# Kernel tuning notes

Hardware: AMD Instinct MI355X
Metric: run time of the kernel (lower is better)

Reference implementation:

```python
import jax, jax.numpy as jnp
import numpy as np

N = 100000           # nodes
E = 1600000          # directed edges (avg degree 16)
G = 64               # graphs in batch


def gcn_conv(x, src, dst, ew, W, b, n):
    """PyG GCNConv with edge weights and self-loops already appended.

    out[i] = sum_{(j->i)} d[j]^-1/2 * ew * d[i]^-1/2 * (x W)[j] + b
    where d[i] = sum of incoming edge weights at i (incl. self-loop).
    """
    xw = x @ W                                               # [n, out]
    deg = jax.ops.segment_sum(ew, dst, num_segments=n)       # [n]
    dinv = jnp.where(deg > 0, jax.lax.rsqrt(deg), 0.0)
    norm = dinv[src] * ew * dinv[dst]                        # [e]
    msg = xw[src] * norm[:, None]                            # [e, out] gather
    out = jax.ops.segment_sum(msg, dst, num_segments=n)      # scatter-add
    return out + b


def setup_inputs() -> dict:
    key = jax.random.key(0)
    ks = jax.random.split(key, 10)
    x = jax.random.normal(ks[0], (N, 256), dtype=jnp.float32)
    edge_index = jax.random.randint(ks[1], (2, E), 0, N, dtype=jnp.int64)
    edge_weight = jax.random.uniform(ks[2], (E,), dtype=jnp.float32)
    batch = jnp.sort(jax.random.randint(ks[3], (N,), 0, G, dtype=jnp.int64))
    s = 0.05
    W1 = jax.random.normal(ks[4], (256, 128), dtype=jnp.float32) * s
    b1 = jnp.zeros((128,), dtype=jnp.float32)
    W2 = jax.random.normal(ks[5], (128, 64), dtype=jnp.float32) * s
    b2 = jnp.zeros((64,), dtype=jnp.float32)
    Wfc = jax.random.normal(ks[6], (64, 1), dtype=jnp.float32) * s
    bfc = jnp.zeros((1,), dtype=jnp.float32)
    return {"x": x, "edge_index": edge_index, "edge_weight": edge_weight,
            "batch": batch, "W1": W1, "b1": b1, "W2": W2, "b2": b2,
            "Wfc": Wfc, "bfc": bfc}


def reference(x, edge_index, edge_weight, batch, W1, b1, W2, b2, Wfc, bfc):
    n = x.shape[0]
    loop = jnp.arange(n, dtype=edge_index.dtype)
    src = jnp.concatenate([edge_index[0], loop])             # add self-loops
    dst = jnp.concatenate([edge_index[1], loop])
    ew = jnp.concatenate([edge_weight, jnp.ones((n,), x.dtype)])

    h = jax.nn.relu(gcn_conv(x, src, dst, ew, W1, b1, n))    # [N,128]
    h = jax.nn.relu(gcn_conv(h, src, dst, ew, W2, b2, n))    # [N,64]

    # global_mean_pool over batch ids
    sums = jax.ops.segment_sum(h, batch, num_segments=G)     # [G,64]
    cnt = jax.ops.segment_sum(jnp.ones((n,), h.dtype), batch, num_segments=G)
    pooled = sums / jnp.maximum(cnt, 1.0)[:, None]
    return pooled @ Wfc + bfc                                # [G,1]
```

## Files before the change

kernel.cpp:

```cpp
#include <hip/hip_runtime.h>
#include <hip/hip_bf16.h>


static inline int ceil_div_ll(long long a, int b) { return (int)((a + b - 1) / b); }

typedef __attribute__((ext_vector_type(8))) short bf16x8;
typedef __attribute__((ext_vector_type(4))) float f32x4;

#define FIX_SCALE 33554432.0f

__device__ inline unsigned short f2bf(float f) {
    __hip_bfloat16 h = __float2bfloat16(f);
    return *reinterpret_cast<unsigned short*>(&h);
}
__device__ inline float bf2f(unsigned short u) {
    unsigned int x = ((unsigned int)u) << 16;
    return __uint_as_float(x);
}

__global__ void k_init_pk(unsigned long long* __restrict__ pk, int n) {
    int i = blockIdx.x * blockDim.x + threadIdx.x;
    if (i < n) pk[i] = (unsigned long long)(1u << 25);
}

__global__ void k_deg_count(const int* __restrict__ dst, const float* __restrict__ ew,
                            unsigned long long* __restrict__ pk, int* __restrict__ slot, int E) {
    int e = blockIdx.x * blockDim.x + threadIdx.x;
    if (e < E) {
        unsigned int fx = __float2uint_rn(ew[e] * FIX_SCALE);
        unsigned long long old =
            atomicAdd(&pk[dst[e]], (1ull << 32) | (unsigned long long)fx);
        slot[e] = (int)(old >> 32);
    }
}

__global__ void k_finish(const unsigned long long* __restrict__ pk, float* __restrict__ dinv,
                         int* __restrict__ count, int n) {
    int i = blockIdx.x * blockDim.x + threadIdx.x;
    if (i < n) {
        unsigned long long v = pk[i];
        float deg = (float)(unsigned int)(v & 0xffffffffull) * (1.0f / FIX_SCALE);
        dinv[i] = (deg > 0.f) ? rsqrtf(deg) : 0.f;
        count[i] = (int)(v >> 32);
    }
}

constexpr int SC_T = 256;
constexpr int SC_PER = 16;
constexpr int SC_CHUNK = SC_T * SC_PER;

__global__ void k_scan_a(const int* __restrict__ count, int* __restrict__ bsum, int n) {
    __shared__ int lds[SC_T];
    int b = blockIdx.x, t = threadIdx.x;
    int base = b * SC_CHUNK + t * SC_PER;
    int s = 0;
#pragma unroll
    for (int k = 0; k < SC_PER; ++k) {
        int idx = base + k;
        if (idx < n) s += count[idx];
    }
    lds[t] = s;
    __syncthreads();
    for (int off = 128; off > 0; off >>= 1) {
        if (t < off) lds[t] += lds[t + off];
        __syncthreads();
    }
    if (t == 0) bsum[b] = lds[0];
}

__global__ void k_scan_b(int* __restrict__ bsum, int nb) {
    if (threadIdx.x == 0) {
        int run = 0;
        for (int i = 0; i < nb; ++i) { int c = bsum[i]; bsum[i] = run; run += c; }
    }
}

__global__ void k_scan_c(const int* __restrict__ count, int* __restrict__ rowptr,
                         const int* __restrict__ bsum, int n) {
    __shared__ int lds[SC_T];
    int b = blockIdx.x, t = threadIdx.x;
    int base = b * SC_CHUNK + t * SC_PER;
    int v[SC_PER];
    int s = 0;
#pragma unroll
    for (int k = 0; k < SC_PER; ++k) {
        int idx = base + k;
        v[k] = (idx < n) ? count[idx] : 0;
        s += v[k];
    }
    lds[t] = s;
    for (int off = 1; off < SC_T; off <<= 1) {
        __syncthreads();
        int tmp = (t >= off) ? lds[t - off] : 0;
        __syncthreads();
        lds[t] += tmp;
    }
    __syncthreads();
    int run = bsum[b] + lds[t] - s;
#pragma unroll
    for (int k = 0; k < SC_PER; ++k) {
        int idx = base + k;
        if (idx < n) {
            rowptr[idx] = run;
            run += v[k];
            if (idx == n - 1) rowptr[n] = run;
        }
    }
}

__global__ void k_csr_fill(const int* __restrict__ src, const int* __restrict__ dst,
                           const float* __restrict__ ew, const float* __restrict__ dinv,
                           const int* __restrict__ rowptr, const int* __restrict__ slot,
                           int2* __restrict__ csr, int E) {
    int e = blockIdx.x * blockDim.x + threadIdx.x;
    if (e < E) {
        int s = src[e], d = dst[e];
        int pos = rowptr[d] + slot[e];
        float coef = dinv[s] * ew[e] * dinv[d];
        csr[pos] = make_int2(s, __float_as_int(coef));
    }
}

template <int KDIM, int ODIM>
__global__ void k_wpack(const float* __restrict__ W, unsigned short* __restrict__ wpk) {
    constexpr int NKS = KDIM / 32, NF = ODIM / 16;
    int t = blockIdx.x * blockDim.x + threadIdx.x;
    if (t >= NKS * NF * 64) return;
    int lane = t & 63;
    int nf   = (t >> 6) % NF;
    int ks   = t / (64 * NF);
    int col  = nf * 16 + (lane & 15);
    int kb   = ks * 32 + (lane >> 4) * 8;
    bf16x8 hi, lo;
#pragma unroll
    for (int i = 0; i < 8; ++i) {
        float w = W[(size_t)(kb + i) * ODIM + col];
        unsigned short h = f2bf(w);
        hi[i] = (short)h;
        lo[i] = (short)f2bf(w - bf2f(h));
    }
    size_t base = (size_t)t * 8;
    *(bf16x8*)(wpk + base) = hi;
    *(bf16x8*)(wpk + (size_t)KDIM * ODIM + base) = lo;
}

template <int KDIM, int ODIM>
__global__ void k_gemm_mfma(const float* __restrict__ X,
                            const unsigned short* __restrict__ wpk,
                            unsigned short* __restrict__ Y, int n) {
    constexpr int NKS = KDIM / 32, NF = ODIM / 16;
    int wid  = threadIdx.x >> 6;
    int lane = threadIdx.x & 63;
    int rowbase = blockIdx.x * 64 + wid * 16;
    int arow = rowbase + (lane & 15);
    int kb0  = (lane >> 4) * 8;
    const unsigned short* wlo = wpk + (size_t)KDIM * ODIM;
    bool aok = (arow < n);
    const float* xr = X + (size_t)arow * KDIM + kb0;

    f32x4 acc[NF];
#pragma unroll
    for (int f = 0; f < NF; ++f) acc[f] = (f32x4){0.f, 0.f, 0.f, 0.f};

#pragma unroll
    for (int ks = 0; ks < NKS; ++ks) {
        f32x4 a0 = (f32x4){0.f, 0.f, 0.f, 0.f};
        f32x4 a1 = (f32x4){0.f, 0.f, 0.f, 0.f};
        if (aok) {
            a0 = *(const f32x4*)(xr + ks * 32);
            a1 = *(const f32x4*)(xr + ks * 32 + 4);
        }
        bf16x8 ahi, alo;
#pragma unroll
        for (int i = 0; i < 4; ++i) {
            unsigned short h0 = f2bf(a0[i]);
            ahi[i]     = (short)h0;
            alo[i]     = (short)f2bf(a0[i] - bf2f(h0));
            unsigned short h1 = f2bf(a1[i]);
            ahi[i + 4] = (short)h1;
            alo[i + 4] = (short)f2bf(a1[i] - bf2f(h1));
        }
#pragma unroll
        for (int f = 0; f < NF; ++f) {
            size_t fb = (((size_t)ks * NF + f) * 64 + lane) * 8;
            bf16x8 bhi = *(const bf16x8*)(wpk + fb);
            bf16x8 blo = *(const bf16x8*)(wlo + fb);
            acc[f] = __builtin_amdgcn_mfma_f32_16x16x32_bf16(ahi, bhi, acc[f], 0, 0, 0);
            acc[f] = __builtin_amdgcn_mfma_f32_16x16x32_bf16(alo, bhi, acc[f], 0, 0, 0);
            acc[f] = __builtin_amdgcn_mfma_f32_16x16x32_bf16(ahi, blo, acc[f], 0, 0, 0);
        }
    }

    int r0  = rowbase + (lane >> 4) * 4;
    int col = lane & 15;
#pragma unroll
    for (int f = 0; f < NF; ++f) {
#pragma unroll
        for (int i = 0; i < 4; ++i) {
            int r = r0 + i;
            if (r < n) Y[(size_t)r * ODIM + f * 16 + col] = f2bf(acc[f][i]);
        }
    }
}

template <int F>
__global__ void k_gather(const unsigned short* __restrict__ xw, const int* __restrict__ rowptr,
                         const int2* __restrict__ csr,
                         const float* __restrict__ dinv, const float* __restrict__ bias,
                         float* __restrict__ out, int n) {
    int wave = threadIdx.x >> 6;
    int lane = threadIdx.x & 63;
    int i = blockIdx.x * 4 + wave;
    if (i >= n) return;

    float dv = dinv[i];
    float sl = dv * dv;
    int e0 = __builtin_amdgcn_readfirstlane(rowptr[i]);
    int e1 = __builtin_amdgcn_readfirstlane(rowptr[i + 1]);

    if constexpr (F == 128) {
        const unsigned int* base = (const unsigned int*)xw;
        unsigned int su = base[(size_t)i * 64 + lane];
        float ax0 = bf2f((unsigned short)(su & 0xffff)) * sl;
        float ay0 = bf2f((unsigned short)(su >> 16)) * sl;
        float ax1 = 0.f, ay1 = 0.f, ax2 = 0.f, ay2 = 0.f, ax3 = 0.f, ay3 = 0.f;
        int e = e0;
        for (; e + 8 <= e1; e += 8) {
            int2 p0 = csr[e + 0], p1 = csr[e + 1], p2 = csr[e + 2], p3 = csr[e + 3];
            int2 p4 = csr[e + 4], p5 = csr[e + 5], p6 = csr[e + 6], p7 = csr[e + 7];
            unsigned int u0 = base[(size_t)p0.x * 64 + lane];
            unsigned int u1 = base[(size_t)p1.x * 64 + lane];
            unsigned int u2 = base[(size_t)p2.x * 64 + lane];
            unsigned int u3 = base[(size_t)p3.x * 64 + lane];
            unsigned int u4 = base[(size_t)p4.x * 64 + lane];
            unsigned int u5 = base[(size_t)p5.x * 64 + lane];
            unsigned int u6 = base[(size_t)p6.x * 64 + lane];
            unsigned int u7 = base[(size_t)p7.x * 64 + lane];
            float c0 = __int_as_float(p0.y), c1 = __int_as_float(p1.y);
            float c2 = __int_as_float(p2.y), c3 = __int_as_float(p3.y);
            float c4 = __int_as_float(p4.y), c5 = __int_as_float(p5.y);
            float c6 = __int_as_float(p6.y), c7 = __int_as_float(p7.y);
            ax0 += c0 * bf2f((unsigned short)(u0 & 0xffff)); ay0 += c0 * bf2f((unsigned short)(u0 >> 16));
            ax1 += c1 * bf2f((unsigned short)(u1 & 0xffff)); ay1 += c1 * bf2f((unsigned short)(u1 >> 16));
            ax2 += c2 * bf2f((unsigned short)(u2 & 0xffff)); ay2 += c2 * bf2f((unsigned short)(u2 >> 16));
            ax3 += c3 * bf2f((unsigned short)(u3 & 0xffff)); ay3 += c3 * bf2f((unsigned short)(u3 >> 16));
            ax0 += c4 * bf2f((unsigned short)(u4 & 0xffff)); ay0 += c4 * bf2f((unsigned short)(u4 >> 16));
            ax1 += c5 * bf2f((unsigned short)(u5 & 0xffff)); ay1 += c5 * bf2f((unsigned short)(u5 >> 16));
            ax2 += c6 * bf2f((unsigned short)(u6 & 0xffff)); ay2 += c6 * bf2f((unsigned short)(u6 >> 16));
            ax3 += c7 * bf2f((unsigned short)(u7 & 0xffff)); ay3 += c7 * bf2f((unsigned short)(u7 >> 16));
        }
        for (; e + 2 <= e1; e += 2) {
            int2 p0 = csr[e + 0], p1 = csr[e + 1];
            unsigned int u0 = base[(size_t)p0.x * 64 + lane];
            unsigned int u1 = base[(size_t)p1.x * 64 + lane];
            float c0 = __int_as_float(p0.y), c1 = __int_as_float(p1.y);
            ax0 += c0 * bf2f((unsigned short)(u0 & 0xffff)); ay0 += c0 * bf2f((unsigned short)(u0 >> 16));
            ax1 += c1 * bf2f((unsigned short)(u1 & 0xffff)); ay1 += c1 * bf2f((unsigned short)(u1 >> 16));
        }
        if (e < e1) {
            int2 p0 = csr[e];
            unsigned int u0 = base[(size_t)p0.x * 64 + lane];
            float c0 = __int_as_float(p0.y);
            ax0 += c0 * bf2f((unsigned short)(u0 & 0xffff)); ay0 += c0 * bf2f((unsigned short)(u0 >> 16));
        }
        float2 bb = *((const float2*)bias + lane);
        float rx = fmaxf((ax0 + ax1) + (ax2 + ax3) + bb.x, 0.f);
        float ry = fmaxf((ay0 + ay1) + (ay2 + ay3) + bb.y, 0.f);
        *((float2*)(out + (size_t)i * F) + lane) = make_float2(rx, ry);
    } else {
        float a0 = bf2f(xw[(size_t)i * 64 + lane]) * sl;
        float a1 = 0.f, a2 = 0.f, a3 = 0.f;
        int e = e0;
        for (; e + 8 <= e1; e += 8) {
            int2 p0 = csr[e + 0], p1 = csr[e + 1], p2 = csr[e + 2], p3 = csr[e + 3];
            int2 p4 = csr[e + 4], p5 = csr[e + 5], p6 = csr[e + 6], p7 = csr[e + 7];
            float v0 = bf2f(xw[(size_t)p0.x * 64 + lane]);
            float v1 = bf2f(xw[(size_t)p1.x * 64 + lane]);
            float v2 = bf2f(xw[(size_t)p2.x * 64 + lane]);
            float v3 = bf2f(xw[(size_t)p3.x * 64 + lane]);
            float v4 = bf2f(xw[(size_t)p4.x * 64 + lane]);
            float v5 = bf2f(xw[(size_t)p5.x * 64 + lane]);
            float v6 = bf2f(xw[(size_t)p6.x * 64 + lane]);
            float v7 = bf2f(xw[(size_t)p7.x * 64 + lane]);
            a0 += __int_as_float(p0.y) * v0; a1 += __int_as_float(p1.y) * v1;
            a2 += __int_as_float(p2.y) * v2; a3 += __int_as_float(p3.y) * v3;
            a0 += __int_as_float(p4.y) * v4; a1 += __int_as_float(p5.y) * v5;
            a2 += __int_as_float(p6.y) * v6; a3 += __int_as_float(p7.y) * v7;
        }
        for (; e + 2 <= e1; e += 2) {
            int2 p0 = csr[e + 0], p1 = csr[e + 1];
            a0 += __int_as_float(p0.y) * bf2f(xw[(size_t)p0.x * 64 + lane]);
            a1 += __int_as_float(p1.y) * bf2f(xw[(size_t)p1.x * 64 + lane]);
        }
        if (e < e1) {
            int2 p0 = csr[e];
            a0 += __int_as_float(p0.y) * bf2f(xw[(size_t)p0.x * 64 + lane]);
        }
        float res = fmaxf((a0 + a1) + (a2 + a3) + bias[lane], 0.f);
        out[(size_t)i * 64 + lane] = res;
    }
}

__global__ void k_fill(float* __restrict__ p, int n, float v) {
    int i = blockIdx.x * blockDim.x + threadIdx.x;
    if (i < n) p[i] = v;
}

__global__ void k_pool1(const float* __restrict__ h2, const int* __restrict__ batch,
                        float* __restrict__ sums, int n) {
    int b = blockIdx.x, t = threadIdx.x;
    int chunk = (n + gridDim.x - 1) / gridDim.x;
    int lo = b * chunk, hi = min(lo + chunk, n);
    if (lo >= hi) return;
    int f = t & 63, rg = t >> 6;
    float acc = 0.f;
    int cur = -1;
    for (int r = lo + rg; r < hi; r += 4) {
        int g = batch[r];
        if (g != cur) {
            if (cur >= 0) atomicAdd(&sums[cur * 64 + f], acc);
            acc = 0.f;
            cur = g;
        }
        acc += h2[(size_t)r * 64 + f];
    }
    if (cur >= 0) atomicAdd(&sums[cur * 64 + f], acc);
}

__global__ void k_head(const float* __restrict__ sums, const int* __restrict__ batch,
                       const float* __restrict__ Wfc, const float* __restrict__ bfc,
                       float* __restrict__ out, int n) {
    int g = blockIdx.x;
    int f = threadIdx.x;
    int lo0 = 0, hi0 = n;
    while (lo0 < hi0) { int m = (lo0 + hi0) >> 1; if (batch[m] < g) lo0 = m + 1; else hi0 = m; }
    int lo1 = lo0, hi1 = n;
    while (lo1 < hi1) { int m = (lo1 + hi1) >> 1; if (batch[m] < g + 1) lo1 = m + 1; else hi1 = m; }
    float cnt = (float)(lo1 - lo0);
    float v = sums[g * 64 + f] * Wfc[f];
#pragma unroll
    for (int o = 32; o > 0; o >>= 1) v += __shfl_down(v, o);
    if (f == 0) out[g] = v / fmaxf(cnt, 1.0f) + bfc[0];
}

extern "C" void kernel_launch(void* const* d_in, const int* in_sizes, int n_in,
                              void* d_out, int out_size, void* d_ws, size_t ws_size,
                              hipStream_t stream) {
    const float* x    = (const float*)d_in[0];
    const int*   ei   = (const int*)d_in[1];
    const float* ew   = (const float*)d_in[2];
    const int*   bat  = (const int*)d_in[3];
    const float* W1   = (const float*)d_in[4];
    const float* b1   = (const float*)d_in[5];
    const float* W2   = (const float*)d_in[6];
    const float* b2   = (const float*)d_in[7];
    const float* Wfc  = (const float*)d_in[8];
    const float* bfc  = (const float*)d_in[9];
    float*       out  = (float*)d_out;

    const int N = in_sizes[0] / 256;
    const int E = in_sizes[2];
    const int G = out_size;

    const int* src = ei;
    const int* dst = ei + E;

    const int NB_SCAN = (N + SC_CHUNK - 1) / SC_CHUNK;

    const int Npad = (N + 4) & ~3;
    unsigned long long* pk       = (unsigned long long*)d_ws;
    float*              dinv     = (float*)(pk + Npad);
    int*                count    = (int*)(dinv + Npad);
    int*                rowptr   = count + Npad;
    int*                bsum     = rowptr + Npad;
    int*                slot     = bsum + ((NB_SCAN + 4) & ~3);
    int2*               csr      = (int2*)(slot + ((E + 4) & ~3));
    unsigned short*     wpk1     = (unsigned short*)(csr + E);
    unsigned short*     wpk2     = wpk1 + 2 * 256 * 128;
    float*              sums     = (float*)(wpk2 + 2 * 128 * 64);
    unsigned short*     bufA     = (unsigned short*)(sums + ((G * 64 + 4) & ~3));
    float*              bufB     = (float*)(bufA + (size_t)N * 128);

    const int B = 256;

    k_init_pk<<<ceil_div_ll(N, B), B, 0, stream>>>(pk, N);
    k_deg_count<<<ceil_div_ll(E, B), B, 0, stream>>>(dst, ew, pk, slot, E);
    k_finish<<<ceil_div_ll(N, B), B, 0, stream>>>(pk, dinv, count, N);

    k_scan_a<<<NB_SCAN, SC_T, 0, stream>>>(count, bsum, N);
    k_scan_b<<<1, 64, 0, stream>>>(bsum, NB_SCAN);
    k_scan_c<<<NB_SCAN, SC_T, 0, stream>>>(count, rowptr, bsum, N);
    k_csr_fill<<<ceil_div_ll(E, B), B, 0, stream>>>(src, dst, ew, dinv, rowptr,
                                                    slot, csr, E);

    k_wpack<256, 128><<<(8 * 8 * 64 + B - 1) / B, B, 0, stream>>>(W1, wpk1);
    k_wpack<128, 64><<<(4 * 4 * 64 + B - 1) / B, B, 0, stream>>>(W2, wpk2);

    k_gemm_mfma<256, 128><<<ceil_div_ll(N, 64), 256, 0, stream>>>(x, wpk1, bufA, N);
    k_gather<128><<<ceil_div_ll(N, 4), 256, 0, stream>>>(
        bufA, rowptr, csr, dinv, b1, bufB, N);

    k_gemm_mfma<128, 64><<<ceil_div_ll(N, 64), 256, 0, stream>>>(bufB, wpk2, bufA, N);
    k_gather<64><<<ceil_div_ll(N, 4), 256, 0, stream>>>(
        bufA, rowptr, csr, dinv, b2, bufB, N);

    k_fill<<<ceil_div_ll(G * 64, B), B, 0, stream>>>(sums, G * 64, 0.0f);
    k_pool1<<<1024, 256, 0, stream>>>(bufB, bat, sums, N);
    k_head<<<G, 64, 0, stream>>>(sums, bat, Wfc, bfc, out, N);
}
```

Baseline: 355.3 us.

## Co-schedule degree atomics with layer-1 GEMM and store hidden layer in bf16

Merges the edge-degree atomic counting kernel and the first MFMA GEMM into one launch, interleaving GEMM blocks among degree blocks by a computed stride so the compute-bound GEMM overlaps the atomic-bound degree pass. The first gather now writes its ReLU output as packed bf16 instead of fp32. The second GEMM reads that bf16 input directly, dropping the hi/lo split of A and using two MFMAs per fragment instead of three. This halves the intermediate write and read traffic, at the cost of some precision in the hidden layer and a mixed-role kernel whose block scheduling is uneven.

```diff
diff --git a/kernel.cpp b/kernel.cpp
--- a/kernel.cpp
+++ b/kernel.cpp
@@ -21,17 +21,6 @@
 __global__ void k_init_pk(unsigned long long* __restrict__ pk, int n) {
     int i = blockIdx.x * blockDim.x + threadIdx.x;
     if (i < n) pk[i] = (unsigned long long)(1u << 25);
-}
-
-__global__ void k_deg_count(const int* __restrict__ dst, const float* __restrict__ ew,
-                            unsigned long long* __restrict__ pk, int* __restrict__ slot, int E) {
-    int e = blockIdx.x * blockDim.x + threadIdx.x;
-    if (e < E) {
-        unsigned int fx = __float2uint_rn(ew[e] * FIX_SCALE);
-        unsigned long long old =
-            atomicAdd(&pk[dst[e]], (1ull << 32) | (unsigned long long)fx);
-        slot[e] = (int)(old >> 32);
-    }
 }
 
 __global__ void k_finish(const unsigned long long* __restrict__ pk, float* __restrict__ dinv,
@@ -145,9 +134,91 @@
 }
 
 template <int KDIM, int ODIM>
-__global__ void k_gemm_mfma(const float* __restrict__ X,
-                            const unsigned short* __restrict__ wpk,
-                            unsigned short* __restrict__ Y, int n) {
+__device__ __forceinline__ void gemm_f32A_body(const float* __restrict__ X,
+                                               const unsigned short* __restrict__ wpk,
+                                               unsigned short* __restrict__ Y, int n, int gb) {
+    constexpr int NKS = KDIM / 32, NF = ODIM / 16;
+    int wid  = threadIdx.x >> 6;
+    int lane = threadIdx.x & 63;
+    int rowbase = gb * 64 + wid * 16;
+    int arow = rowbase + (lane & 15);
+    int kb0  = (lane >> 4) * 8;
+    const unsigned short* wlo = wpk + (size_t)KDIM * ODIM;
+    bool aok = (arow < n);
+    const float* xr = X + (size_t)arow * KDIM + kb0;
+
+    f32x4 acc[NF];
+#pragma unroll
+    for (int f = 0; f < NF; ++f) acc[f] = (f32x4){0.f, 0.f, 0.f, 0.f};
+
+#pragma unroll
+    for (int ks = 0; ks < NKS; ++ks) {
+        f32x4 a0 = (f32x4){0.f, 0.f, 0.f, 0.f};
+        f32x4 a1 = (f32x4){0.f, 0.f, 0.f, 0.f};
+        if (aok) {
+            a0 = *(const f32x4*)(xr + ks * 32);
+            a1 = *(const f32x4*)(xr + ks * 32 + 4);
+        }
+        bf16x8 ahi, alo;
+#pragma unroll
+        for (int i = 0; i < 4; ++i) {
+            unsigned short h0 = f2bf(a0[i]);
+            ahi[i]     = (short)h0;
+            alo[i]     = (short)f2bf(a0[i] - bf2f(h0));
+            unsigned short h1 = f2bf(a1[i]);
+            ahi[i + 4] = (short)h1;
+            alo[i + 4] = (short)f2bf(a1[i] - bf2f(h1));
+        }
+#pragma unroll
+        for (int f = 0; f < NF; ++f) {
+            size_t fb = (((size_t)ks * NF + f) * 64 + lane) * 8;
+            bf16x8 bhi = *(const bf16x8*)(wpk + fb);
+            bf16x8 blo = *(const bf16x8*)(wlo + fb);
+            acc[f] = __builtin_amdgcn_mfma_f32_16x16x32_bf16(ahi, bhi, acc[f], 0, 0, 0);
+            acc[f] = __builtin_amdgcn_mfma_f32_16x16x32_bf16(alo, bhi, acc[f], 0, 0, 0);
+            acc[f] = __builtin_amdgcn_mfma_f32_16x16x32_bf16(ahi, blo, acc[f], 0, 0, 0);
+        }
+    }
+
+    int r0  = rowbase + (lane >> 4) * 4;
+    int col = lane & 15;
+#pragma unroll
+    for (int f = 0; f < NF; ++f) {
+#pragma unroll
+        for (int i = 0; i < 4; ++i) {
+            int r = r0 + i;
+            if (r < n) Y[(size_t)r * ODIM + f * 16 + col] = f2bf(acc[f][i]);
+        }
+    }
+}
+
+__global__ void k_deg_gemm1(const int* __restrict__ dst, const float* __restrict__ ew,
+                            unsigned long long* __restrict__ pk, int* __restrict__ slot, int E,
+                            const float* __restrict__ X, const unsigned short* __restrict__ wpk,
+                            unsigned short* __restrict__ Y, int n,
+                            int gemmBlocks, int stride) {
+    int bid = blockIdx.x;
+    int q = bid / stride;
+    bool isGemm = (bid % stride == 0) && (q < gemmBlocks);
+    if (isGemm) {
+        gemm_f32A_body<256, 128>(X, wpk, Y, n, q);
+    } else {
+        int nGemmBefore = min(q + 1, gemmBlocks);
+        int db = bid - nGemmBefore;
+        int e = db * 256 + (int)threadIdx.x;
+        if (e < E) {
+            unsigned int fx = __float2uint_rn(ew[e] * FIX_SCALE);
+            unsigned long long old =
+                atomicAdd(&pk[dst[e]], (1ull << 32) | (unsigned long long)fx);
+            slot[e] = (int)(old >> 32);
+        }
+    }
+}
+
+template <int KDIM, int ODIM>
+__global__ void k_gemm_mfma_bfA(const unsigned short* __restrict__ X,
+                                const unsigned short* __restrict__ wpk,
+                                unsigned short* __restrict__ Y, int n) {
     constexpr int NKS = KDIM / 32, NF = ODIM / 16;
     int wid  = threadIdx.x >> 6;
     int lane = threadIdx.x & 63;
@@ -156,7 +227,7 @@
     int kb0  = (lane >> 4) * 8;
     const unsigned short* wlo = wpk + (size_t)KDIM * ODIM;
     bool aok = (arow < n);
-    const float* xr = X + (size_t)arow * KDIM + kb0;
+    const unsigned short* xr = X + (size_t)arow * KDIM + kb0;
 
     f32x4 acc[NF];
 #pragma unroll
@@ -164,30 +235,15 @@
 
 #pragma unroll
     for (int ks = 0; ks < NKS; ++ks) {
-        f32x4 a0 = (f32x4){0.f, 0.f, 0.f, 0.f};
-        f32x4 a1 = (f32x4){0.f, 0.f, 0.f, 0.f};
-        if (aok) {
-            a0 = *(const f32x4*)(xr + ks * 32);
-            a1 = *(const f32x4*)(xr + ks * 32 + 4);
-        }
-        bf16x8 ahi, alo;
-#pragma unroll
-        for (int i = 0; i < 4; ++i) {
-            unsigned short h0 = f2bf(a0[i]);
-            ahi[i]     = (short)h0;
-            alo[i]     = (short)f2bf(a0[i] - bf2f(h0));
-            unsigned short h1 = f2bf(a1[i]);
-            ahi[i + 4] = (short)h1;
-            alo[i + 4] = (short)f2bf(a1[i] - bf2f(h1));
-        }
+        bf16x8 a = (bf16x8){0, 0, 0, 0, 0, 0, 0, 0};
+        if (aok) a = *(const bf16x8*)(xr + ks * 32);
 #pragma unroll
         for (int f = 0; f < NF; ++f) {
             size_t fb = (((size_t)ks * NF + f) * 64 + lane) * 8;
             bf16x8 bhi = *(const bf16x8*)(wpk + fb);
             bf16x8 blo = *(const bf16x8*)(wlo + fb);
-            acc[f] = __builtin_amdgcn_mfma_f32_16x16x32_bf16(ahi, bhi, acc[f], 0, 0, 0);
-            acc[f] = __builtin_amdgcn_mfma_f32_16x16x32_bf16(alo, bhi, acc[f], 0, 0, 0);
-            acc[f] = __builtin_amdgcn_mfma_f32_16x16x32_bf16(ahi, blo, acc[f], 0, 0, 0);
+            acc[f] = __builtin_amdgcn_mfma_f32_16x16x32_bf16(a, bhi, acc[f], 0, 0, 0);
+            acc[f] = __builtin_amdgcn_mfma_f32_16x16x32_bf16(a, blo, acc[f], 0, 0, 0);
         }
     }
 
@@ -203,11 +259,10 @@
     }
 }
 
-template <int F>
-__global__ void k_gather(const unsigned short* __restrict__ xw, const int* __restrict__ rowptr,
-                         const int2* __restrict__ csr,
-                         const float* __restrict__ dinv, const float* __restrict__ bias,
-                         float* __restrict__ out, int n) {
+__global__ void k_gather1(const unsigned short* __restrict__ xw, const int* __restrict__ rowptr,
+                          const int2* __restrict__ csr,
+                          const float* __restrict__ dinv, const float* __restrict__ bias,
+                          unsigned short* __restrict__ out, int n) {
     int wave = threadIdx.x >> 6;
     int lane = threadIdx.x & 63;
     int i = blockIdx.x * 4 + wave;
@@ -218,87 +273,101 @@
     int e0 = __builtin_amdgcn_readfirstlane(rowptr[i]);
     int e1 = __builtin_amdgcn_readfirstlane(rowptr[i + 1]);
 
-    if constexpr (F == 128) {
-        const unsigned int* base = (const unsigned int*)xw;
-        unsigned int su = base[(size_t)i * 64 + lane];
-        float ax0 = bf2f((unsigned short)(su & 0xffff)) * sl;
-        float ay0 = bf2f((unsigned short)(su >> 16)) * sl;
-        float ax1 = 0.f, ay1 = 0.f, ax2 = 0.f, ay2 = 0.f, ax3 = 0.f, ay3 = 0.f;
-        int e = e0;
-        for (; e + 8 <= e1; e += 8) {
-            int2 p0 = csr[e + 0], p1 = csr[e + 1], p2 = csr[e + 2], p3 = csr[e + 3];
-            int2 p4 = csr[e + 4], p5 = csr[e + 5], p6 = csr[e + 6], p7 = csr[e + 7];
-            unsigned int u0 = base[(size_t)p0.x * 64 + lane];
-            unsigned int u1 = base[(size_t)p1.x * 64 + lane];
-            unsigned int u2 = base[(size_t)p2.x * 64 + lane];
-            unsigned int u3 = base[(size_t)p3.x * 64 + lane];
-            unsigned int u4 = base[(size_t)p4.x * 64 + lane];
-            unsigned int u5 = base[(size_t)p5.x * 64 + lane];
-            unsigned int u6 = base[(size_t)p6.x * 64 + lane];
-            unsigned int u7 = base[(size_t)p7.x * 64 + lane];
-            float c0 = __int_as_float(p0.y), c1 = __int_as_float(p1.y);
-            float c2 = __int_as_float(p2.y), c3 = __int_as_float(p3.y);
-            float c4 = __int_as_float(p4.y), c5 = __int_as_float(p5.y);
-            float c6 = __int_as_float(p6.y), c7 = __int_as_float(p7.y);
-            ax0 += c0 * bf2f((unsigned short)(u0 & 0xffff)); ay0 += c0 * bf2f((unsigned short)(u0 >> 16));
-            ax1 += c1 * bf2f((unsigned short)(u1 & 0xffff)); ay1 += c1 * bf2f((unsigned short)(u1 >> 16));
-            ax2 += c2 * bf2f((unsigned short)(u2 & 0xffff)); ay2 += c2 * bf2f((unsigned short)(u2 >> 16));
-            ax3 += c3 * bf2f((unsigned short)(u3 & 0xffff)); ay3 += c3 * bf2f((unsigned short)(u3 >> 16));
-            ax0 += c4 * bf2f((unsigned short)(u4 & 0xffff)); ay0 += c4 * bf2f((unsigned short)(u4 >> 16));
-            ax1 += c5 * bf2f((unsigned short)(u5 & 0xffff)); ay1 += c5 * bf2f((unsigned short)(u5 >> 16));
-            ax2 += c6 * bf2f((unsigned short)(u6 & 0xffff)); ay2 += c6 * bf2f((unsigned short)(u6 >> 16));
-            ax3 += c7 * bf2f((unsigned short)(u7 & 0xffff)); ay3 += c7 * bf2f((unsigned short)(u7 >> 16));
-        }
-        for (; e + 2 <= e1; e += 2) {
-            int2 p0 = csr[e + 0], p1 = csr[e + 1];
-            unsigned int u0 = base[(size_t)p0.x * 64 + lane];
-            unsigned int u1 = base[(size_t)p1.x * 64 + lane];
-            float c0 = __int_as_float(p0.y), c1 = __int_as_float(p1.y);
-            ax0 += c0 * bf2f((unsigned short)(u0 & 0xffff)); ay0 += c0 * bf2f((unsigned short)(u0 >> 16));
-            ax1 += c1 * bf2f((unsigned short)(u1 & 0xffff)); ay1 += c1 * bf2f((unsigned short)(u1 >> 16));
-        }
-        if (e < e1) {
-            int2 p0 = csr[e];
-            unsigned int u0 = base[(size_t)p0.x * 64 + lane];
-            float c0 = __int_as_float(p0.y);
-            ax0 += c0 * bf2f((unsigned short)(u0 & 0xffff)); ay0 += c0 * bf2f((unsigned short)(u0 >> 16));
-        }
-        float2 bb = *((const float2*)bias + lane);
-        float rx = fmaxf((ax0 + ax1) + (ax2 + ax3) + bb.x, 0.f);
-        float ry = fmaxf((ay0 + ay1) + (ay2 + ay3) + bb.y, 0.f);
-        *((float2*)(out + (size_t)i * F) + lane) = make_float2(rx, ry);
-    } else {
-        float a0 = bf2f(xw[(size_t)i * 64 + lane]) * sl;
-        float a1 = 0.f, a2 = 0.f, a3 = 0.f;
-        int e = e0;
-        for (; e + 8 <= e1; e += 8) {
-            int2 p0 = csr[e + 0], p1 = csr[e + 1], p2 = csr[e + 2], p3 = csr[e + 3];
-            int2 p4 = csr[e + 4], p5 = csr[e + 5], p6 = csr[e + 6], p7 = csr[e + 7];
-            float v0 = bf2f(xw[(size_t)p0.x * 64 + lane]);
-            float v1 = bf2f(xw[(size_t)p1.x * 64 + lane]);
-            float v2 = bf2f(xw[(size_t)p2.x * 64 + lane]);
-            float v3 = bf2f(xw[(size_t)p3.x * 64 + lane]);
-            float v4 = bf2f(xw[(size_t)p4.x * 64 + lane]);
-            float v5 = bf2f(xw[(size_t)p5.x * 64 + lane]);
-            float v6 = bf2f(xw[(size_t)p6.x * 64 + lane]);
-            float v7 = bf2f(xw[(size_t)p7.x * 64 + lane]);
-            a0 += __int_as_float(p0.y) * v0; a1 += __int_as_float(p1.y) * v1;
-            a2 += __int_as_float(p2.y) * v2; a3 += __int_as_float(p3.y) * v3;
-            a0 += __int_as_float(p4.y) * v4; a1 += __int_as_float(p5.y) * v5;
-            a2 += __int_as_float(p6.y) * v6; a3 += __int_as_float(p7.y) * v7;
-        }
-        for (; e + 2 <= e1; e += 2) {
-            int2 p0 = csr[e + 0], p1 = csr[e + 1];
-            a0 += __int_as_float(p0.y) * bf2f(xw[(size_t)p0.x * 64 + lane]);
-            a1 += __int_as_float(p1.y) * bf2f(xw[(size_t)p1.x * 64 + lane]);
-        }
-        if (e < e1) {
-            int2 p0 = csr[e];
-            a0 += __int_as_float(p0.y) * bf2f(xw[(size_t)p0.x * 64 + lane]);
-        }
-        float res = fmaxf((a0 + a1) + (a2 + a3) + bias[lane], 0.f);
-        out[(size_t)i * 64 + lane] = res;
-    }
+    const unsigned int* base = (const unsigned int*)xw;
+    unsigned int su = base[(size_t)i * 64 + lane];
+    float ax0 = bf2f((unsigned short)(su & 0xffff)) * sl;
+    float ay0 = bf2f((unsigned short)(su >> 16)) * sl;
+    float ax1 = 0.f, ay1 = 0.f, ax2 = 0.f, ay2 = 0.f, ax3 = 0.f, ay3 = 0.f;
+    int e = e0;
+    for (; e + 8 <= e1; e += 8) {
+        int2 p0 = csr[e + 0], p1 = csr[e + 1], p2 = csr[e + 2], p3 = csr[e + 3];
+        int2 p4 = csr[e + 4], p5 = csr[e + 5], p6 = csr[e + 6], p7 = csr[e + 7];
+        unsigned int u0 = base[(size_t)p0.x * 64 + lane];
+        unsigned int u1 = base[(size_t)p1.x * 64 + lane];
+        unsigned int u2 = base[(size_t)p2.x * 64 + lane];
+        unsigned int u3 = base[(size_t)p3.x * 64 + lane];
+        unsigned int u4 = base[(size_t)p4.x * 64 + lane];
+        unsigned int u5 = base[(size_t)p5.x * 64 + lane];
+        unsigned int u6 = base[(size_t)p6.x * 64 + lane];
+        unsigned int u7 = base[(size_t)p7.x * 64 + lane];
+        float c0 = __int_as_float(p0.y), c1 = __int_as_float(p1.y);
+        float c2 = __int_as_float(p2.y), c3 = __int_as_float(p3.y);
+        float c4 = __int_as_float(p4.y), c5 = __int_as_float(p5.y);
+        float c6 = __int_as_float(p6.y), c7 = __int_as_float(p7.y);
+        ax0 += c0 * bf2f((unsigned short)(u0 & 0xffff)); ay0 += c0 * bf2f((unsigned short)(u0 >> 16));
+        ax1 += c1 * bf2f((unsigned short)(u1 & 0xffff)); ay1 += c1 * bf2f((unsigned short)(u1 >> 16));
+        ax2 += c2 * bf2f((unsigned short)(u2 & 0xffff)); ay2 += c2 * bf2f((unsigned short)(u2 >> 16));
+        ax3 += c3 * bf2f((unsigned short)(u3 & 0xffff)); ay3 += c3 * bf2f((unsigned short)(u3 >> 16));
+        ax0 += c4 * bf2f((unsigned short)(u4 & 0xffff)); ay0 += c4 * bf2f((unsigned short)(u4 >> 16));
+        ax1 += c5 * bf2f((unsigned short)(u5 & 0xffff)); ay1 += c5 * bf2f((unsigned short)(u5 >> 16));
+        ax2 += c6 * bf2f((unsigned short)(u6 & 0xffff)); ay2 += c6 * bf2f((unsigned short)(u6 >> 16));
+        ax3 += c7 * bf2f((unsigned short)(u7 & 0xffff)); ay3 += c7 * bf2f((unsigned short)(u7 >> 16));
+    }
+    for (; e + 2 <= e1; e += 2) {
+        int2 p0 = csr[e + 0], p1 = csr[e + 1];
+        unsigned int u0 = base[(size_t)p0.x * 64 + lane];
+        unsigned int u1 = base[(size_t)p1.x * 64 + lane];
+        float c0 = __int_as_float(p0.y), c1 = __int_as_float(p1.y);
+        ax0 += c0 * bf2f((unsigned short)(u0 & 0xffff)); ay0 += c0 * bf2f((unsigned short)(u0 >> 16));
+        ax1 += c1 * bf2f((unsigned short)(u1 & 0xffff)); ay1 += c1 * bf2f((unsigned short)(u1 >> 16));
+    }
+    if (e < e1) {
+        int2 p0 = csr[e];
+        unsigned int u0 = base[(size_t)p0.x * 64 + lane];
+        float c0 = __int_as_float(p0.y);
+        ax0 += c0 * bf2f((unsigned short)(u0 & 0xffff)); ay0 += c0 * bf2f((unsigned short)(u0 >> 16));
+    }
+    float2 bb = *((const float2*)bias + lane);
+    float rx = fmaxf((ax0 + ax1) + (ax2 + ax3) + bb.x, 0.f);
+    float ry = fmaxf((ay0 + ay1) + (ay2 + ay3) + bb.y, 0.f);
+    unsigned int packed = (unsigned int)f2bf(rx) | ((unsigned int)f2bf(ry) << 16);
+    ((unsigned int*)(out + (size_t)i * 128))[lane] = packed;
+}
+
+__global__ void k_gather2(const unsigned short* __restrict__ xw, const int* __restrict__ rowptr,
+                          const int2* __restrict__ csr,
+                          const float* __restrict__ dinv, const float* __restrict__ bias,
+                          float* __restrict__ out, int n) {
+    int wave = threadIdx.x >> 6;
+    int lane = threadIdx.x & 63;
+    int i = blockIdx.x * 4 + wave;
+    if (i >= n) return;
+
+    float dv = dinv[i];
+    float sl = dv * dv;
+    int e0 = __builtin_amdgcn_readfirstlane(rowptr[i]);
+    int e1 = __builtin_amdgcn_readfirstlane(rowptr[i + 1]);
+
+    float a0 = bf2f(xw[(size_t)i * 64 + lane]) * sl;
+    float a1 = 0.f, a2 = 0.f, a3 = 0.f;
+    int e = e0;
+    for (; e + 8 <= e1; e += 8) {
+        int2 p0 = csr[e + 0], p1 = csr[e + 1], p2 = csr[e + 2], p3 = csr[e + 3];
+        int2 p4 = csr[e + 4], p5 = csr[e + 5], p6 = csr[e + 6], p7 = csr[e + 7];
+        float v0 = bf2f(xw[(size_t)p0.x * 64 + lane]);
+        float v1 = bf2f(xw[(size_t)p1.x * 64 + lane]);
+        float v2 = bf2f(xw[(size_t)p2.x * 64 + lane]);
+        float v3 = bf2f(xw[(size_t)p3.x * 64 + lane]);
+        float v4 = bf2f(xw[(size_t)p4.x * 64 + lane]);
+        float v5 = bf2f(xw[(size_t)p5.x * 64 + lane]);
+        float v6 = bf2f(xw[(size_t)p6.x * 64 + lane]);
+        float v7 = bf2f(xw[(size_t)p7.x * 64 + lane]);
+        a0 += __int_as_float(p0.y) * v0; a1 += __int_as_float(p1.y) * v1;
+        a2 += __int_as_float(p2.y) * v2; a3 += __int_as_float(p3.y) * v3;
+        a0 += __int_as_float(p4.y) * v4; a1 += __int_as_float(p5.y) * v5;
+        a2 += __int_as_float(p6.y) * v6; a3 += __int_as_float(p7.y) * v7;
+    }
+    for (; e + 2 <= e1; e += 2) {
+        int2 p0 = csr[e + 0], p1 = csr[e + 1];
+        a0 += __int_as_float(p0.y) * bf2f(xw[(size_t)p0.x * 64 + lane]);
+        a1 += __int_as_float(p1.y) * bf2f(xw[(size_t)p1.x * 64 + lane]);
+    }
+    if (e < e1) {
+        int2 p0 = csr[e];
+        a0 += __int_as_float(p0.y) * bf2f(xw[(size_t)p0.x * 64 + lane]);
+    }
+    float res = fmaxf((a0 + a1) + (a2 + a3) + bias[lane], 0.f);
+    out[(size_t)i * 64 + lane] = res;
 }
 
 __global__ void k_fill(float* __restrict__ p, int n, float v) {
@@ -368,23 +437,35 @@
     const int NB_SCAN = (N + SC_CHUNK - 1) / SC_CHUNK;
 
     const int Npad = (N + 4) & ~3;
-    unsigned long long* pk       = (unsigned long long*)d_ws;
-    float*              dinv     = (float*)(pk + Npad);
-    int*                count    = (int*)(dinv + Npad);
-    int*                rowptr   = count + Npad;
-    int*                bsum     = rowptr + Npad;
-    int*                slot     = bsum + ((NB_SCAN + 4) & ~3);
-    int2*               csr      = (int2*)(slot + ((E + 4) & ~3));
-    unsigned short*     wpk1     = (unsigned short*)(csr + E);
-    unsigned short*     wpk2     = wpk1 + 2 * 256 * 128;
-    float*              sums     = (float*)(wpk2 + 2 * 128 * 64);
-    unsigned short*     bufA     = (unsigned short*)(sums + ((G * 64 + 4) & ~3));
-    float*              bufB     = (float*)(bufA + (size_t)N * 128);
+    unsigned long long* pk     = (unsigned long long*)d_ws;
+    float*              dinv   = (float*)(pk + Npad);
+    int*                count  = (int*)(dinv + Npad);
+    int*                rowptr = count + Npad;
+    int*                bsum   = rowptr + Npad;
+    int*                slot   = bsum + ((NB_SCAN + 4) & ~3);
+    int2*               csr    = (int2*)(slot + ((E + 4) & ~3));
+    unsigned short*     wpk1   = (unsigned short*)(csr + E);
+    unsigned short*     wpk2   = wpk1 + 2 * 256 * 128;
+    float*              sums   = (float*)(wpk2 + 2 * 128 * 64);
+    unsigned short*     bufA   = (unsigned short*)(sums + ((G * 64 + 4) & ~3));
+    unsigned short*     bufH1  = bufA + (size_t)N * 128;
+    float*              bufH2  = (float*)(bufH1 + (size_t)N * 128);
 
     const int B = 256;
 
     k_init_pk<<<ceil_div_ll(N, B), B, 0, stream>>>(pk, N);
-    k_deg_count<<<ceil_div_ll(E, B), B, 0, stream>>>(dst, ew, pk, slot, E);
+    k_wpack<256, 128><<<(8 * 8 * 64 + B - 1) / B, B, 0, stream>>>(W1, wpk1);
+    k_wpack<128, 64><<<(4 * 4 * 64 + B - 1) / B, B, 0, stream>>>(W2, wpk2);
+
+    {
+        int degBlocks  = ceil_div_ll(E, B);
+        int gemmBlocks = ceil_div_ll(N, 64);
+        int total      = degBlocks + gemmBlocks;
+        int stride     = total / gemmBlocks;
+        if (stride < 1) stride = 1;
+        k_deg_gemm1<<<total, B, 0, stream>>>(dst, ew, pk, slot, E,
+                                             x, wpk1, bufA, N, gemmBlocks, stride);
+    }
     k_finish<<<ceil_div_ll(N, B), B, 0, stream>>>(pk, dinv, count, N);
 
     k_scan_a<<<NB_SCAN, SC_T, 0, stream>>>(count, bsum, N);
@@ -393,18 +474,14 @@
     k_csr_fill<<<ceil_div_ll(E, B), B, 0, stream>>>(src, dst, ew, dinv, rowptr,
                                                     slot, csr, E);
 
-    k_wpack<256, 128><<<(8 * 8 * 64 + B - 1) / B, B, 0, stream>>>(W1, wpk1);
-    k_wpack<128, 64><<<(4 * 4 * 64 + B - 1) / B, B, 0, stream>>>(W2, wpk2);
-
-    k_gemm_mfma<256, 128><<<ceil_div_ll(N, 64), 256, 0, stream>>>(x, wpk1, bufA, N);
-    k_gather<128><<<ceil_div_ll(N, 4), 256, 0, stream>>>(
-        bufA, rowptr, csr, dinv, b1, bufB, N);
-
-    k_gemm_mfma<128, 64><<<ceil_div_ll(N, 64), 256, 0, stream>>>(bufB, wpk2, bufA, N);
-    k_gather<64><<<ceil_div_ll(N, 4), 256, 0, stream>>>(
-        bufA, rowptr, csr, dinv, b2, bufB, N);
+    k_gather1<<<ceil_div_ll(N, 4), 256, 0, stream>>>(
+        bufA, rowptr, csr, dinv, b1, bufH1, N);
+
+    k_gemm_mfma_bfA<128, 64><<<ceil_div_ll(N, 64), 256, 0, stream>>>(bufH1, wpk2, bufA, N);
+    k_gather2<<<ceil_div_ll(N, 4), 256, 0, stream>>>(
+        bufA, rowptr, csr, dinv, b2, bufH2, N);
 
     k_fill<<<ceil_div_ll(G * 64, B), B, 0, stream>>>(sums, G * 64, 0.0f);
-    k_pool1<<<1024, 256, 0, stream>>>(bufB, bat, sums, N);
+    k_pool1<<<1024, 256, 0, stream>>>(bufH2, bat, sums, N);
     k_head<<<G, 64, 0, stream>>>(sums, bat, Wfc, bfc, out, N);
 }
```

After: 409.0 us. +15.1%, slower.
